# Kernel optimization log

Measured on AMD Instinct MI355X. Metric: run time of the kernel, lower is better.

Reference implementation:

```python
import jax, jax.numpy as jnp
import numpy as np

B, S, D, H = 2, 2048, 768, 12
DH = D // H  # 64

def setup_inputs() -> dict:
    key = jax.random.key(0)
    ks = jax.random.split(key, 5)
    x = jax.random.normal(ks[0], (B, S, D), dtype=jnp.float32)
    # causal mask: True = attend (lower triangular), bool -> constant w.r.t. grads
    attn_mask = jnp.tril(jnp.ones((S, S), dtype=bool))[None, None, :, :]
    c_attn_w = jax.random.normal(ks[1], (D, 3 * D), dtype=jnp.float32) * 0.02
    c_attn_b = jnp.zeros((3 * D,), dtype=jnp.float32)
    c_proj_w = jax.random.normal(ks[2], (D, D), dtype=jnp.float32) * 0.02
    c_proj_b = jnp.zeros((D,), dtype=jnp.float32)
    return {"x": x, "attn_mask": attn_mask, "c_attn_w": c_attn_w,
            "c_attn_b": c_attn_b, "c_proj_w": c_proj_w, "c_proj_b": c_proj_b}

def reference(x, attn_mask, c_attn_w, c_attn_b, c_proj_w, c_proj_b):
    # qkv projection (Conv1D == addmm)
    qkv = x @ c_attn_w + c_attn_b                      # [B,S,3D]
    q, k, v = jnp.split(qkv, 3, axis=-1)               # each [B,S,D]
    def split_heads(t):
        return t.reshape(B, S, H, DH).transpose(0, 2, 1, 3)  # [B,H,S,DH]
    q, k, v = split_heads(q), split_heads(k), split_heads(v)
    scores = jnp.einsum('bhqd,bhkd->bhqk', q, k) / jnp.sqrt(jnp.float32(DH))
    neg = jnp.asarray(-1e9, dtype=scores.dtype)
    scores = jnp.where(attn_mask, scores, neg)         # additive causal mask
    probs = jax.nn.softmax(scores, axis=-1)            # dropout: eval mode (identity)
    out = jnp.einsum('bhqk,bhkd->bhqd', probs, v)      # [B,H,S,DH]
    out = out.transpose(0, 2, 1, 3).reshape(B, S, D)   # merge heads
    return out @ c_proj_w + c_proj_b
```

## Files before the change

### kernel.cpp

```cpp
#include <hip/hip_runtime.h>
#include <cstddef>
#include <cstdint>

#define Bsz  2
#define Ssz  2048
#define Dsz  768
#define Hsz  12
#define DHsz 64
#define Msz  4096
#define N3sz 2304
#define Kdim 768

typedef short bf16x8 __attribute__((ext_vector_type(8)));
typedef short bf16x4 __attribute__((ext_vector_type(4)));
typedef float f32x4  __attribute__((ext_vector_type(4)));
typedef const __attribute__((address_space(1))) void gvoid;
typedef __attribute__((address_space(3))) void lvoid;

static __device__ __forceinline__ unsigned short f2bf(float f) {
    unsigned int u = __builtin_bit_cast(unsigned int, f);
    u += 0x7FFFu + ((u >> 16) & 1u);
    return (unsigned short)(u >> 16);
}
static __device__ __forceinline__ unsigned int pk2bf(float a, float b) {
    return (unsigned int)f2bf(a) | ((unsigned int)f2bf(b) << 16);
}

static __device__ __forceinline__ void transpose_body(
    const float* __restrict__ W, unsigned short* __restrict__ Wt, int N,
    int bx, int by, int tid, float (*T)[65])
{
    const int n0 = bx << 6;
    const int k0 = by << 6;
#pragma unroll
    for (int p = 0; p < 4; ++p) {
        const int idx = p * 256 + tid;
        const int r  = idx >> 4;
        const int c4 = (idx & 15) << 2;
        const float4 v = *(const float4*)&W[(size_t)(k0 + r) * N + n0 + c4];
        T[r][c4 + 0] = v.x; T[r][c4 + 1] = v.y;
        T[r][c4 + 2] = v.z; T[r][c4 + 3] = v.w;
    }
    __syncthreads();
#pragma unroll
    for (int p = 0; p < 4; ++p) {
        const int idx = p * 256 + tid;
        const int r  = idx >> 4;
        const int c4 = (idx & 15) << 2;
        ushort4 o;
        o.x = f2bf(T[c4 + 0][r]); o.y = f2bf(T[c4 + 1][r]);
        o.z = f2bf(T[c4 + 2][r]); o.w = f2bf(T[c4 + 3][r]);
        *(ushort4*)&Wt[(size_t)(n0 + r) * Kdim + k0 + c4] = o;
    }
}

__global__ __launch_bounds__(256) void prep_kernel(
    const float* __restrict__ X, unsigned short* __restrict__ Xb,
    const float* __restrict__ Wqkv, unsigned short* __restrict__ Wqkvt,
    const float* __restrict__ Wproj, unsigned short* __restrict__ Wprojt)
{
    __shared__ float T[64][65];
    const int bid = blockIdx.x;
    const int tid = threadIdx.x;
    if (bid < 1536) {
        const size_t i = ((size_t)bid * 256 + tid) * 8;
        const float4 a = *(const float4*)&X[i];
        const float4 b = *(const float4*)&X[i + 4];
        ushort4 lo, hi;
        lo.x = f2bf(a.x); lo.y = f2bf(a.y); lo.z = f2bf(a.z); lo.w = f2bf(a.w);
        hi.x = f2bf(b.x); hi.y = f2bf(b.y); hi.z = f2bf(b.z); hi.w = f2bf(b.w);
        *(ushort4*)&Xb[i] = lo;
        *(ushort4*)&Xb[i + 4] = hi;
    } else if (bid < 1536 + 432) {
        const int idx = bid - 1536;
        transpose_body(Wqkv, Wqkvt, N3sz, idx % 36, idx / 36, tid, T);
    } else {
        const int idx = bid - 1968;
        transpose_body(Wproj, Wprojt, Dsz, idx % 12, idx / 12, tid, T);
    }
}

__global__ __launch_bounds__(256) void qkv_gemm_kernel(
    const unsigned short* __restrict__ A,
    const unsigned short* __restrict__ Bt,
    const float* __restrict__ bias,
    unsigned short* __restrict__ Qo, unsigned short* __restrict__ Ko,
    unsigned short* __restrict__ Vo)
{
    __shared__ unsigned short smem[128 * 136];
    unsigned short* Als = smem;
    unsigned short* Bls = smem + 8192;

    const int tid  = threadIdx.x;
    const int w    = tid >> 6;
    const int lane = tid & 63;
    const int quad = lane >> 4;
    const int t16  = lane & 15;
    const int wm   = w & 1;
    const int wn   = w >> 1;
    const int m0   = blockIdx.y << 7;
    const int n0   = blockIdx.x << 7;

    const int lrow = lane >> 3;
    const int lch  = lane & 7;
    const unsigned short* Ag = A  + (size_t)(m0 + lrow) * Kdim + ((lch ^ lrow) << 3);
    const unsigned short* Bg = Bt + (size_t)(n0 + lrow) * Kdim + ((lch ^ lrow) << 3);

    f32x4 acc[4][4];
#pragma unroll
    for (int mt = 0; mt < 4; ++mt)
#pragma unroll
        for (int nt = 0; nt < 4; ++nt) acc[mt][nt] = (f32x4)(0.f);

    for (int k0 = 0; k0 < Kdim; k0 += 64) {
        __syncthreads();
#pragma unroll
        for (int t = 0; t < 4; ++t) {
            const int i = (w << 2) + t;
            __builtin_amdgcn_global_load_lds(
                (gvoid*)(Ag + (size_t)(i << 3) * Kdim + k0),
                (lvoid*)(Als + (i << 9)), 16, 0, 0);
            __builtin_amdgcn_global_load_lds(
                (gvoid*)(Bg + (size_t)(i << 3) * Kdim + k0),
                (lvoid*)(Bls + (i << 9)), 16, 0, 0);
        }
        __syncthreads();

#pragma unroll
        for (int ks = 0; ks < 2; ++ks) {
            const int sl = (((ks << 2) + quad) ^ (t16 & 7)) << 3;
            bf16x8 af[4], bfr[4];
#pragma unroll
            for (int mt = 0; mt < 4; ++mt)
                af[mt] = *(const bf16x8*)&Als[(((wm << 6) + (mt << 4) + t16) << 6) + sl];
#pragma unroll
            for (int nt = 0; nt < 4; ++nt)
                bfr[nt] = *(const bf16x8*)&Bls[(((wn << 6) + (nt << 4) + t16) << 6) + sl];
#pragma unroll
            for (int mt = 0; mt < 4; ++mt)
#pragma unroll
                for (int nt = 0; nt < 4; ++nt)
                    acc[mt][nt] = __builtin_amdgcn_mfma_f32_16x16x32_bf16(
                        bfr[nt], af[mt], acc[mt][nt], 0, 0, 0);
        }
    }

    __syncthreads();
    {
        const int seg = n0 / Dsz;
        const float sc = (seg == 0) ? 0.18033688f : 1.0f;
#pragma unroll
        for (int nt = 0; nt < 4; ++nt) {
            const int nl = (wn << 6) + (nt << 4) + (quad << 2);
            const float4 bn = *(const float4*)&bias[n0 + nl];
#pragma unroll
            for (int mt = 0; mt < 4; ++mt) {
                const int ml = (wm << 6) + (mt << 4) + t16;
                uint2 o;
                o.x = pk2bf((acc[mt][nt][0] + bn.x) * sc,
                            (acc[mt][nt][1] + bn.y) * sc);
                o.y = pk2bf((acc[mt][nt][2] + bn.z) * sc,
                            (acc[mt][nt][3] + bn.w) * sc);
                *(uint2*)&smem[ml * 136 + nl] = o;
            }
        }
        __syncthreads();
        unsigned short* dst0 = (seg == 0) ? Qo : (seg == 1) ? Ko : Vo;
        const int h0 = (n0 % Dsz) >> 6;
        const int chunk = tid & 7;
#pragma unroll
        for (int p = 0; p < 8; ++p) {
            const int unit = p * 32 + (tid >> 3);
            const int ml = unit >> 1;
            const int hc = unit & 1;
            const int m  = m0 + ml;
            const int bI = m >> 11;
            const int s  = m & 2047;
            const uint4 v = *(const uint4*)&smem[ml * 136 + (hc << 6) + (chunk << 3)];
            *(uint4*)&dst0[(((size_t)bI * Hsz + h0 + hc) * Ssz + s) * DHsz
                           + (chunk << 3)] = v;
        }
    }
}

__global__ __launch_bounds__(256) void proj_gemm_kernel(
    const unsigned short* __restrict__ A,
    const unsigned short* __restrict__ Bt,
    const float* __restrict__ bias, float* __restrict__ Out)
{
    __shared__ float smemf[64 * 68];
    unsigned short* Als = (unsigned short*)smemf;
    unsigned short* Bls = Als + 4096;

    const int tid  = threadIdx.x;
    const int w    = tid >> 6;
    const int lane = tid & 63;
    const int quad = lane >> 4;
    const int t16  = lane & 15;
    const int wm   = w & 1;
    const int wn   = w >> 1;
    const int m0   = blockIdx.y << 6;
    const int n0   = blockIdx.x << 6;

    const int lrow = lane >> 3;
    const int lch  = lane & 7;
    const unsigned short* Ag = A  + (size_t)(m0 + lrow) * Kdim + ((lch ^ lrow) << 3);
    const unsigned short* Bg = Bt + (size_t)(n0 + lrow) * Kdim + ((lch ^ lrow) << 3);

    f32x4 acc[2][2];
#pragma unroll
    for (int mt = 0; mt < 2; ++mt)
#pragma unroll
        for (int nt = 0; nt < 2; ++nt) acc[mt][nt] = (f32x4)(0.f);

    for (int k0 = 0; k0 < Kdim; k0 += 64) {
        __syncthreads();
#pragma unroll
        for (int t = 0; t < 2; ++t) {
            const int i = (w << 1) + t;
            __builtin_amdgcn_global_load_lds(
                (gvoid*)(Ag + (size_t)(i << 3) * Kdim + k0),
                (lvoid*)(Als + (i << 9)), 16, 0, 0);
            __builtin_amdgcn_global_load_lds(
                (gvoid*)(Bg + (size_t)(i << 3) * Kdim + k0),
                (lvoid*)(Bls + (i << 9)), 16, 0, 0);
        }
        __syncthreads();

#pragma unroll
        for (int ks = 0; ks < 2; ++ks) {
            const int sl = (((ks << 2) + quad) ^ (t16 & 7)) << 3;
            bf16x8 af[2], bfr[2];
#pragma unroll
            for (int mt = 0; mt < 2; ++mt)
                af[mt] = *(const bf16x8*)&Als[(((wm << 5) + (mt << 4) + t16) << 6) + sl];
#pragma unroll
            for (int nt = 0; nt < 2; ++nt)
                bfr[nt] = *(const bf16x8*)&Bls[(((wn << 5) + (nt << 4) + t16) << 6) + sl];
#pragma unroll
            for (int mt = 0; mt < 2; ++mt)
#pragma unroll
                for (int nt = 0; nt < 2; ++nt)
                    acc[mt][nt] = __builtin_amdgcn_mfma_f32_16x16x32_bf16(
                        bfr[nt], af[mt], acc[mt][nt], 0, 0, 0);
        }
    }

    __syncthreads();
#pragma unroll
    for (int nt = 0; nt < 2; ++nt) {
        const int nl = (wn << 5) + (nt << 4) + (quad << 2);
        const float4 bn = *(const float4*)&bias[n0 + nl];
#pragma unroll
        for (int mt = 0; mt < 2; ++mt) {
            const int ml = (wm << 5) + (mt << 4) + t16;
            float4 o;
            o.x = acc[mt][nt][0] + bn.x;
            o.y = acc[mt][nt][1] + bn.y;
            o.z = acc[mt][nt][2] + bn.z;
            o.w = acc[mt][nt][3] + bn.w;
            *(float4*)&smemf[ml * 68 + nl] = o;
        }
    }
    __syncthreads();
    {
        const int c16 = tid & 15;
#pragma unroll
        for (int p = 0; p < 4; ++p) {
            const int ml = p * 16 + (tid >> 4);
            const float4 v = *(const float4*)&smemf[ml * 68 + (c16 << 2)];
            *(float4*)&Out[(size_t)(m0 + ml) * Dsz + n0 + (c16 << 2)] = v;
        }
    }
}

__global__ __launch_bounds__(256) void attn_mfma_kernel(
    const unsigned short* __restrict__ Q, const unsigned short* __restrict__ K,
    const unsigned short* __restrict__ V, unsigned short* __restrict__ Aout)
{
    __shared__ unsigned short Kls[2][64 * 72];
    __shared__ unsigned short Vls[2][64 * 72];

    const int tid  = threadIdx.x;
    const int w    = tid >> 6;
    const int lane = tid & 63;
    const int quad = lane >> 4;
    const int t16  = lane & 15;

    const int c    = blockIdx.x & 255;
    const int slot = blockIdx.x >> 8;
    const int u    = (slot == 0) ? c : (slot == 1) ? (511 - c) : (512 + c);
    const int qt   = 31 - (u / 24);
    const int bh   = u % 24;
    const int q0   = qt << 6;
    const int bIdx = bh / Hsz;
    const int h    = bh % Hsz;

    const size_t base = (size_t)bh * Ssz * DHsz;

    const int kv_a = tid >> 3;
    const int kc_a = tid & 7;
    const int kvp  = tid & 31;
    const int dc   = tid >> 5;

    bf16x8 qf[2];
#pragma unroll
    for (int s = 0; s < 2; ++s)
        qf[s] = *(const bf16x8*)&Q[base + (size_t)(q0 + w * 16 + t16) * DHsz
                                   + s * 32 + quad * 8];

    f32x4 O[4];
    float l_ps = 0.f;
#pragma unroll
    for (int dt = 0; dt < 4; ++dt) O[dt] = (f32x4)(0.f);

    {
        const unsigned short* Kb = K + base;
        const unsigned short* Vb = V + base;
        const uint4 k0a = *(const uint4*)&Kb[(size_t)kv_a * DHsz + kc_a * 8];
        const uint4 k0b = *(const uint4*)&Kb[(size_t)(kv_a + 32) * DHsz + kc_a * 8];
        const uint4 v0a = *(const uint4*)&Vb[(size_t)(2 * kvp) * DHsz + dc * 8];
        const uint4 v0b = *(const uint4*)&Vb[(size_t)(2 * kvp + 1) * DHsz + dc * 8];
        *(uint4*)&Kls[0][kv_a * 72 + kc_a * 8] = k0a;
        *(uint4*)&Kls[0][(kv_a + 32) * 72 + kc_a * 8] = k0b;
        const unsigned short* pa = reinterpret_cast<const unsigned short*>(&v0a);
        const unsigned short* pb = reinterpret_cast<const unsigned short*>(&v0b);
#pragma unroll
        for (int j = 0; j < 8; ++j) {
            const unsigned int pk = (unsigned int)pa[j] | ((unsigned int)pb[j] << 16);
            *(unsigned int*)&Vls[0][(dc * 8 + j) * 72 + 2 * kvp] = pk;
        }
    }
    __syncthreads();

    for (int kt = 0; kt <= qt; ++kt) {
        const int cur = kt & 1;
        const int nxt = cur ^ 1;

        uint4 kr0, kr1, va, vb;
        if (kt < qt) {
            const unsigned short* Kb = K + base + (size_t)((kt + 1) << 6) * DHsz;
            const unsigned short* Vb = V + base + (size_t)((kt + 1) << 6) * DHsz;
            kr0 = *(const uint4*)&Kb[(size_t)kv_a * DHsz + kc_a * 8];
            kr1 = *(const uint4*)&Kb[(size_t)(kv_a + 32) * DHsz + kc_a * 8];
            va  = *(const uint4*)&Vb[(size_t)(2 * kvp) * DHsz + dc * 8];
            vb  = *(const uint4*)&Vb[(size_t)(2 * kvp + 1) * DHsz + dc * 8];
        }

        f32x4 St[4];
#pragma unroll
        for (int kb = 0; kb < 4; ++kb) St[kb] = (f32x4)(0.f);
#pragma unroll
        for (int s = 0; s < 2; ++s)
#pragma unroll
            for (int kb = 0; kb < 4; ++kb) {
                const bf16x8 kf = *(const bf16x8*)&Kls[cur][(kb * 16 + t16) * 72
                                                           + s * 32 + quad * 8];
                St[kb] = __builtin_amdgcn_mfma_f32_16x16x32_bf16(kf, qf[s], St[kb], 0, 0, 0);
            }

        if (kt == qt) {
            const int qrel = w * 16 + t16;
#pragma unroll
            for (int kb = 0; kb < 4; ++kb) {
                const int kvb = kb * 16 + quad * 4;
#pragma unroll
                for (int r = 0; r < 4; ++r)
                    if (kvb + r > qrel) St[kb][r] = -1e30f;
            }
        }

#pragma unroll
        for (int kb = 0; kb < 4; ++kb) {
            const float p0 = exp2f(St[kb][0]);
            const float p1 = exp2f(St[kb][1]);
            const float p2 = exp2f(St[kb][2]);
            const float p3 = exp2f(St[kb][3]);
            l_ps += (p0 + p1) + (p2 + p3);
            uint2 pk;
            pk.x = pk2bf(p0, p1);
            pk.y = pk2bf(p2, p3);
            const bf16x4 pf = __builtin_bit_cast(bf16x4, pk);
#pragma unroll
            for (int dt = 0; dt < 4; ++dt) {
                const bf16x4 vf = *(const bf16x4*)&Vls[cur][(dt * 16 + t16) * 72
                                                            + kb * 16 + quad * 4];
                O[dt] = __builtin_amdgcn_mfma_f32_16x16x16bf16_1k(vf, pf, O[dt], 0, 0, 0);
            }
        }

        if (kt < qt) {
            *(uint4*)&Kls[nxt][kv_a * 72 + kc_a * 8] = kr0;
            *(uint4*)&Kls[nxt][(kv_a + 32) * 72 + kc_a * 8] = kr1;
            const unsigned short* pa = reinterpret_cast<const unsigned short*>(&va);
            const unsigned short* pb = reinterpret_cast<const unsigned short*>(&vb);
#pragma unroll
            for (int j = 0; j < 8; ++j) {
                const unsigned int pk = (unsigned int)pa[j] | ((unsigned int)pb[j] << 16);
                *(unsigned int*)&Vls[nxt][(dc * 8 + j) * 72 + 2 * kvp] = pk;
            }
            __syncthreads();
        }
    }

    l_ps += __shfl_xor(l_ps, 16);
    l_ps += __shfl_xor(l_ps, 32);
    {
        const float inv = 1.0f / l_ps;
        const int q = q0 + w * 16 + t16;
        unsigned short* dst = Aout + ((size_t)bIdx * Ssz + q) * Dsz + (h << 6);
#pragma unroll
        for (int dt = 0; dt < 4; ++dt) {
            uint2 o;
            o.x = pk2bf(O[dt][0] * inv, O[dt][1] * inv);
            o.y = pk2bf(O[dt][2] * inv, O[dt][3] * inv);
            *(uint2*)&dst[dt * 16 + quad * 4] = o;
        }
    }
}

extern "C" void kernel_launch(void* const* d_in, const int* in_sizes, int n_in,
                              void* d_out, int out_size, void* d_ws, size_t ws_size,
                              hipStream_t stream) {
    const float* x        = (const float*)d_in[0];
    const float* c_attn_w = (const float*)d_in[2];
    const float* c_attn_b = (const float*)d_in[3];
    const float* c_proj_w = (const float*)d_in[4];
    const float* c_proj_b = (const float*)d_in[5];
    float* out = (float*)d_out;

    const size_t T = (size_t)Msz * Dsz;
    unsigned short* xb     = (unsigned short*)d_ws;
    unsigned short* Wqkvt  = xb + T;
    unsigned short* Wprojt = Wqkvt + (size_t)N3sz * Kdim;
    unsigned short* Qw     = Wprojt + (size_t)Dsz * Kdim;
    unsigned short* Kw     = Qw + T;
    unsigned short* Vw     = Kw + T;
    unsigned short* Ab     = Vw + T;

    prep_kernel<<<2112, 256, 0, stream>>>(x, xb, c_attn_w, Wqkvt, c_proj_w, Wprojt);
    qkv_gemm_kernel<<<dim3(N3sz / 128, Msz / 128), 256, 0, stream>>>(
        xb, Wqkvt, c_attn_b, Qw, Kw, Vw);
    attn_mfma_kernel<<<32 * 24, 256, 0, stream>>>(Qw, Kw, Vw, Ab);
    proj_gemm_kernel<<<dim3(Dsz / 64, Msz / 64), 256, 0, stream>>>(
        Ab, Wprojt, c_proj_b, out);
}
```

Baseline: 167.9 us.

## Write V transposed from QKV GEMM epilogue to simplify attention V loads

The QKV GEMM epilogue now stores V in a [B,H,DH,S] transposed layout by gathering columns from shared memory, so the attention kernel can load V tiles with plain 16-byte copies into LDS. This removes the per-tile scalar repacking of V (eight 32-bit LDS stores per thread) from the attention inner loop. In exchange the GEMM epilogue does strided 16-bit LDS reads across rows, which may cause bank conflicts and adds work there.

```diff
diff --git a/kernel.cpp b/kernel.cpp
--- a/kernel.cpp
+++ b/kernel.cpp
@@ -85,7 +85,7 @@
     const unsigned short* __restrict__ Bt,
     const float* __restrict__ bias,
     unsigned short* __restrict__ Qo, unsigned short* __restrict__ Ko,
-    unsigned short* __restrict__ Vo)
+    unsigned short* __restrict__ Vt)
 {
     __shared__ unsigned short smem[128 * 136];
     unsigned short* Als = smem;
@@ -165,20 +165,42 @@
             }
         }
         __syncthreads();
-        unsigned short* dst0 = (seg == 0) ? Qo : (seg == 1) ? Ko : Vo;
+
         const int h0 = (n0 % Dsz) >> 6;
-        const int chunk = tid & 7;
-#pragma unroll
-        for (int p = 0; p < 8; ++p) {
-            const int unit = p * 32 + (tid >> 3);
-            const int ml = unit >> 1;
-            const int hc = unit & 1;
-            const int m  = m0 + ml;
-            const int bI = m >> 11;
-            const int s  = m & 2047;
-            const uint4 v = *(const uint4*)&smem[ml * 136 + (hc << 6) + (chunk << 3)];
-            *(uint4*)&dst0[(((size_t)bI * Hsz + h0 + hc) * Ssz + s) * DHsz
-                           + (chunk << 3)] = v;
+        const int bI = m0 >> 11;
+        const int s0 = m0 & 2047;
+        if (seg < 2) {
+            unsigned short* dst0 = (seg == 0) ? Qo : Ko;
+            const int chunk = tid & 7;
+#pragma unroll
+            for (int p = 0; p < 8; ++p) {
+                const int unit = p * 32 + (tid >> 3);
+                const int ml = unit >> 1;
+                const int hc = unit & 1;
+                const int s  = s0 + ml;
+                const uint4 v = *(const uint4*)&smem[ml * 136 + (hc << 6) + (chunk << 3)];
+                *(uint4*)&dst0[(((size_t)bI * Hsz + h0 + hc) * Ssz + s) * DHsz
+                               + (chunk << 3)] = v;
+            }
+        } else {
+            const int nrow = tid >> 1;
+            const int mh   = tid & 1;
+            const int d    = nrow & 63;
+            const int hc   = nrow >> 6;
+            unsigned short* dst = Vt
+                + ((size_t)(bI * Hsz + h0 + hc) * DHsz + d) * Ssz + s0 + (mh << 6);
+#pragma unroll
+            for (int c = 0; c < 4; ++c) {
+                unsigned int dw[8];
+#pragma unroll
+                for (int k = 0; k < 8; ++k) {
+                    const int j = c * 16 + 2 * k;
+                    dw[k] = (unsigned int)smem[((mh << 6) + j) * 136 + nrow]
+                          | ((unsigned int)smem[((mh << 6) + j + 1) * 136 + nrow] << 16);
+                }
+                *(uint4*)&dst[c * 16]     = make_uint4(dw[0], dw[1], dw[2], dw[3]);
+                *(uint4*)&dst[c * 16 + 8] = make_uint4(dw[4], dw[5], dw[6], dw[7]);
+            }
         }
     }
 }
@@ -276,7 +298,7 @@
 
 __global__ __launch_bounds__(256) void attn_mfma_kernel(
     const unsigned short* __restrict__ Q, const unsigned short* __restrict__ K,
-    const unsigned short* __restrict__ V, unsigned short* __restrict__ Aout)
+    const unsigned short* __restrict__ Vt, unsigned short* __restrict__ Aout)
 {
     __shared__ unsigned short Kls[2][64 * 72];
     __shared__ unsigned short Vls[2][64 * 72];
@@ -296,12 +318,11 @@
     const int bIdx = bh / Hsz;
     const int h    = bh % Hsz;
 
-    const size_t base = (size_t)bh * Ssz * DHsz;
-
-    const int kv_a = tid >> 3;
-    const int kc_a = tid & 7;
-    const int kvp  = tid & 31;
-    const int dc   = tid >> 5;
+    const size_t base  = (size_t)bh * Ssz * DHsz;
+    const size_t vbase = (size_t)bh * DHsz * Ssz;
+
+    const int row_a = tid >> 3;
+    const int ch_a  = tid & 7;
 
     bf16x8 qf[2];
 #pragma unroll
@@ -316,20 +337,15 @@
 
     {
         const unsigned short* Kb = K + base;
-        const unsigned short* Vb = V + base;
-        const uint4 k0a = *(const uint4*)&Kb[(size_t)kv_a * DHsz + kc_a * 8];
-        const uint4 k0b = *(const uint4*)&Kb[(size_t)(kv_a + 32) * DHsz + kc_a * 8];
-        const uint4 v0a = *(const uint4*)&Vb[(size_t)(2 * kvp) * DHsz + dc * 8];
-        const uint4 v0b = *(const uint4*)&Vb[(size_t)(2 * kvp + 1) * DHsz + dc * 8];
-        *(uint4*)&Kls[0][kv_a * 72 + kc_a * 8] = k0a;
-        *(uint4*)&Kls[0][(kv_a + 32) * 72 + kc_a * 8] = k0b;
-        const unsigned short* pa = reinterpret_cast<const unsigned short*>(&v0a);
-        const unsigned short* pb = reinterpret_cast<const unsigned short*>(&v0b);
-#pragma unroll
-        for (int j = 0; j < 8; ++j) {
-            const unsigned int pk = (unsigned int)pa[j] | ((unsigned int)pb[j] << 16);
-            *(unsigned int*)&Vls[0][(dc * 8 + j) * 72 + 2 * kvp] = pk;
-        }
+        const unsigned short* Vb = Vt + vbase;
+        const uint4 k0a = *(const uint4*)&Kb[(size_t)row_a * DHsz + ch_a * 8];
+        const uint4 k0b = *(const uint4*)&Kb[(size_t)(row_a + 32) * DHsz + ch_a * 8];
+        const uint4 v0a = *(const uint4*)&Vb[(size_t)row_a * Ssz + ch_a * 8];
+        const uint4 v0b = *(const uint4*)&Vb[(size_t)(row_a + 32) * Ssz + ch_a * 8];
+        *(uint4*)&Kls[0][row_a * 72 + ch_a * 8] = k0a;
+        *(uint4*)&Kls[0][(row_a + 32) * 72 + ch_a * 8] = k0b;
+        *(uint4*)&Vls[0][row_a * 72 + ch_a * 8] = v0a;
+        *(uint4*)&Vls[0][(row_a + 32) * 72 + ch_a * 8] = v0b;
     }
     __syncthreads();
 
@@ -337,14 +353,14 @@
         const int cur = kt & 1;
         const int nxt = cur ^ 1;
 
-        uint4 kr0, kr1, va, vb;
+        uint4 kr0, kr1, vr0, vr1;
         if (kt < qt) {
             const unsigned short* Kb = K + base + (size_t)((kt + 1) << 6) * DHsz;
-            const unsigned short* Vb = V + base + (size_t)((kt + 1) << 6) * DHsz;
-            kr0 = *(const uint4*)&Kb[(size_t)kv_a * DHsz + kc_a * 8];
-            kr1 = *(const uint4*)&Kb[(size_t)(kv_a + 32) * DHsz + kc_a * 8];
-            va  = *(const uint4*)&Vb[(size_t)(2 * kvp) * DHsz + dc * 8];
-            vb  = *(const uint4*)&Vb[(size_t)(2 * kvp + 1) * DHsz + dc * 8];
+            const unsigned short* Vb = Vt + vbase + ((kt + 1) << 6);
+            kr0 = *(const uint4*)&Kb[(size_t)row_a * DHsz + ch_a * 8];
+            kr1 = *(const uint4*)&Kb[(size_t)(row_a + 32) * DHsz + ch_a * 8];
+            vr0 = *(const uint4*)&Vb[(size_t)row_a * Ssz + ch_a * 8];
+            vr1 = *(const uint4*)&Vb[(size_t)(row_a + 32) * Ssz + ch_a * 8];
         }
 
         f32x4 St[4];
@@ -390,15 +406,10 @@
         }
 
         if (kt < qt) {
-            *(uint4*)&Kls[nxt][kv_a * 72 + kc_a * 8] = kr0;
-            *(uint4*)&Kls[nxt][(kv_a + 32) * 72 + kc_a * 8] = kr1;
-            const unsigned short* pa = reinterpret_cast<const unsigned short*>(&va);
-            const unsigned short* pb = reinterpret_cast<const unsigned short*>(&vb);
-#pragma unroll
-            for (int j = 0; j < 8; ++j) {
-                const unsigned int pk = (unsigned int)pa[j] | ((unsigned int)pb[j] << 16);
-                *(unsigned int*)&Vls[nxt][(dc * 8 + j) * 72 + 2 * kvp] = pk;
-            }
+            *(uint4*)&Kls[nxt][row_a * 72 + ch_a * 8] = kr0;
+            *(uint4*)&Kls[nxt][(row_a + 32) * 72 + ch_a * 8] = kr1;
+            *(uint4*)&Vls[nxt][row_a * 72 + ch_a * 8] = vr0;
+            *(uint4*)&Vls[nxt][(row_a + 32) * 72 + ch_a * 8] = vr1;
             __syncthreads();
         }
     }
```

Result: faster. 164.3 us (-2.1%).
